# Kernel optimization log

Measured on AMD Instinct MI355X. Metric: run time of the kernel, lower is better.

Reference implementation:

```python
import jax, jax.numpy as jnp
import numpy as np

D = 1024
NH = 16
HD = D // NH
DFF = 4 * D
EPS = 1e-5


def setup_inputs() -> dict:
    key = jax.random.key(0)
    ks = jax.random.split(key, 12)
    s = lambda fan_in: 1.0 / np.sqrt(fan_in)
    return {
        "x": jax.random.normal(ks[0], (2, 2048, D), dtype=jnp.float32),
        # weights stored [in, out] (transpose of torch Linear layout)
        "w_qkv": jax.random.uniform(ks[1], (D, 3 * D), minval=-s(D), maxval=s(D)),
        "w_proj": jax.random.uniform(ks[2], (D, D), minval=-s(D), maxval=s(D)),
        "ln1_w": jnp.ones((D,), jnp.float32),
        "ln1_b": jnp.zeros((D,), jnp.float32),
        "ln2_w": jnp.ones((D,), jnp.float32),
        "ln2_b": jnp.zeros((D,), jnp.float32),
        "fc1_w": jax.random.uniform(ks[3], (D, DFF), minval=-s(D), maxval=s(D)),
        "fc1_b": jax.random.uniform(ks[4], (DFF,), minval=-s(D), maxval=s(D)),
        "fc2_w": jax.random.uniform(ks[5], (DFF, D), minval=-s(DFF), maxval=s(DFF)),
        "fc2_b": jax.random.uniform(ks[6], (D,), minval=-s(DFF), maxval=s(DFF)),
    }


def _layernorm(x, w, b):
    mu = jnp.mean(x, axis=-1, keepdims=True)
    var = jnp.mean(jnp.square(x - mu), axis=-1, keepdims=True)
    return (x - mu) * jax.lax.rsqrt(var + EPS) * w + b


def _attn(x, w_qkv, w_proj):
    B, T, C = x.shape
    qkv = x @ w_qkv  # [B,T,3C]
    q, k, v = jnp.split(qkv, 3, axis=-1)
    q = q.reshape(B, T, NH, HD).transpose(0, 2, 1, 3)  # [B,nh,T,hd]
    k = k.reshape(B, T, NH, HD).transpose(0, 2, 1, 3)
    v = v.reshape(B, T, NH, HD).transpose(0, 2, 1, 3)
    att = jnp.einsum("bhqd,bhkd->bhqk", q, k) / np.sqrt(HD)
    causal = jnp.tril(jnp.ones((T, T), bool))
    att = jnp.where(causal, att, -jnp.inf)
    att = jax.nn.softmax(att, axis=-1)
    out = jnp.einsum("bhqk,bhkd->bhqd", att, v)
    out = out.transpose(0, 2, 1, 3).reshape(B, T, C)
    return out @ w_proj


def reference(x, w_qkv, w_proj, ln1_w, ln1_b, ln2_w, ln2_b, fc1_w, fc1_b, fc2_w, fc2_b):
    x = x + _attn(_layernorm(x, ln1_w, ln1_b), w_qkv, w_proj)
    h = _layernorm(x, ln2_w, ln2_b)
    h = jax.nn.gelu(h @ fc1_w + fc1_b, approximate=False) @ fc2_w + fc2_b
    return x + h
```

## Files before the change

kernel.cpp:

```cpp
#include <hip/hip_runtime.h>


typedef short  bf16x8 __attribute__((ext_vector_type(8)));
typedef short  bf16x4 __attribute__((ext_vector_type(4)));
typedef float  fx4    __attribute__((ext_vector_type(4)));
typedef int    ix2    __attribute__((ext_vector_type(2)));

#define DEV static __device__ __forceinline__

DEV short f2bf(float f) {
    unsigned u = __builtin_bit_cast(unsigned, f);
    u += 0x7fffu + ((u >> 16) & 1u);
    return (short)(u >> 16);
}

#define AS1(p) ((__attribute__((address_space(1))) void*)(p))
#define AS3(p) ((__attribute__((address_space(3))) void*)(p))

__global__ __launch_bounds__(256) void ln_kernel(const float* __restrict__ x,
                                                 const float* __restrict__ w,
                                                 const float* __restrict__ b,
                                                 short* __restrict__ out)
{
    int row = blockIdx.x;
    int tid = threadIdx.x;
    const float4 v = *(const float4*)(x + (size_t)row * 1024 + tid * 4);
    float s = v.x + v.y + v.z + v.w;
    float q = v.x * v.x + v.y * v.y + v.z * v.z + v.w * v.w;
#pragma unroll
    for (int off = 32; off > 0; off >>= 1) {
        s += __shfl_down(s, off);
        q += __shfl_down(q, off);
    }
    __shared__ float ls[4], lq[4];
    if ((tid & 63) == 0) { ls[tid >> 6] = s; lq[tid >> 6] = q; }
    __syncthreads();
    float S  = ls[0] + ls[1] + ls[2] + ls[3];
    float Q  = lq[0] + lq[1] + lq[2] + lq[3];
    float mu  = S * (1.0f / 1024.0f);
    float var = Q * (1.0f / 1024.0f) - mu * mu;
    float inv = rsqrtf(var + 1e-5f);
    float4 wv = *(const float4*)(w + tid * 4);
    float4 bv = *(const float4*)(b + tid * 4);
    bf16x4 o;
    o[0] = f2bf((v.x - mu) * inv * wv.x + bv.x);
    o[1] = f2bf((v.y - mu) * inv * wv.y + bv.y);
    o[2] = f2bf((v.z - mu) * inv * wv.z + bv.z);
    o[3] = f2bf((v.w - mu) * inv * wv.w + bv.w);
    *(bf16x4*)(out + (size_t)row * 1024 + tid * 4) = o;
}

__global__ void transpose_f32_bf16(const float* __restrict__ in,
                                   short* __restrict__ out, int R, int C)
{
    __shared__ float tile[32][33];
    int c0 = blockIdx.x * 32, r0 = blockIdx.y * 32;
    int tx = threadIdx.x, ty = threadIdx.y;
#pragma unroll
    for (int dy = 0; dy < 32; dy += 8)
        tile[ty + dy][tx] = in[(size_t)(r0 + ty + dy) * C + c0 + tx];
    __syncthreads();
#pragma unroll
    for (int dy = 0; dy < 32; dy += 8)
        out[(size_t)(c0 + ty + dy) * R + r0 + tx] = f2bf(tile[tx][ty + dy]);
}

__global__ void vt_extract(const short* __restrict__ qkv, short* __restrict__ vt)
{
    __shared__ short tile[32][33];
    int t0 = blockIdx.x * 32, d0 = blockIdx.y * 32;
    int bh = blockIdx.z;
    int tx = threadIdx.x, ty = threadIdx.y;
    size_t inbase  = (size_t)(bh >> 4) * 2048 * 3072 + 2048 + (bh & 15) * 64;
    size_t outbase = (size_t)bh * 64 * 2048;
#pragma unroll
    for (int dy = 0; dy < 32; dy += 8)
        tile[ty + dy][tx] = qkv[inbase + (size_t)(t0 + ty + dy) * 3072 + d0 + tx];
    __syncthreads();
#pragma unroll
    for (int dy = 0; dy < 32; dy += 8)
        vt[outbase + (size_t)(d0 + ty + dy) * 2048 + t0 + tx] = tile[tx][ty + dy];
}

template <int BN, bool BIAS, bool GELU, bool RESID, bool OUT_BF16, bool PARTIAL>
__global__ __launch_bounds__(256) void gemm_bt(const short* __restrict__ A,
                                               const short* __restrict__ Bt,
                                               void* __restrict__ Cout,
                                               void* __restrict__ Cout2,
                                               const float* __restrict__ bias,
                                               const float* __restrict__ resid,
                                               int M, int N, int K)
{
    constexpr int NJ = BN / 32;
    __shared__ short As[2][128 * 32];
    __shared__ short Bs[2][BN * 32];
    int tid  = threadIdx.x;
    int lane = tid & 63, wv = tid >> 6;
    int quad = lane >> 4, l15 = lane & 15;
    int m0 = blockIdx.y * 128, n0 = blockIdx.x * BN;
    int SK   = gridDim.z;
    int kbeg = blockIdx.z * (K / SK);
    int NK   = (K / SK) / 32;
    int wr = (wv >> 1) * 64, wc = (wv & 1) * (BN / 2);
    fx4 acc[4][NJ] = {};
    int srow = lane >> 2;
    int scol = ((lane & 3) ^ (srow & 3)) * 8;
    int rg   = (quad ^ (l15 & 3)) * 8;
    const short* Ab = A  + (size_t)m0 * K;
    const short* Bb = Bt + (size_t)n0 * K;

    auto stage = [&](int buf, int k0) {
#pragma unroll
        for (int c = wv; c < 8; c += 4) {
            int row = c * 16 + srow;
            __builtin_amdgcn_global_load_lds(AS1(Ab + (size_t)row * K + k0 + scol),
                                             AS3(&As[buf][c * 512]), 16, 0, 0);
        }
#pragma unroll
        for (int c = wv; c < BN / 16; c += 4) {
            int row = c * 16 + srow;
            __builtin_amdgcn_global_load_lds(AS1(Bb + (size_t)row * K + k0 + scol),
                                             AS3(&Bs[buf][c * 512]), 16, 0, 0);
        }
    };

    stage(0, kbeg);
    __syncthreads();
    for (int kt = 0; kt < NK; ++kt) {
        int cur = kt & 1;
        if (kt + 1 < NK) stage(cur ^ 1, kbeg + (kt + 1) * 32);
        bf16x8 af[4], bfr[NJ];
#pragma unroll
        for (int i = 0; i < 4; ++i)
            af[i] = *(const bf16x8*)&As[cur][(wr + i * 16 + l15) * 32 + rg];
#pragma unroll
        for (int j = 0; j < NJ; ++j)
            bfr[j] = *(const bf16x8*)&Bs[cur][(wc + j * 16 + l15) * 32 + rg];
#pragma unroll
        for (int i = 0; i < 4; ++i)
#pragma unroll
            for (int j = 0; j < NJ; ++j)
                acc[i][j] = __builtin_amdgcn_mfma_f32_16x16x32_bf16(af[i], bfr[j], acc[i][j], 0, 0, 0);
        __syncthreads();
    }

    if constexpr (PARTIAL) {
        float* P = blockIdx.z ? (float*)Cout2 : (float*)Cout;
#pragma unroll
        for (int i = 0; i < 4; ++i)
#pragma unroll
            for (int j = 0; j < NJ; ++j)
#pragma unroll
                for (int r = 0; r < 4; ++r) {
                    int row = m0 + wr + i * 16 + quad * 4 + r;
                    int col = n0 + wc + j * 16 + l15;
                    P[(size_t)row * N + col] = acc[i][j][r];
                }
    } else {
#pragma unroll
        for (int i = 0; i < 4; ++i)
#pragma unroll
            for (int j = 0; j < NJ; ++j)
#pragma unroll
                for (int r = 0; r < 4; ++r) {
                    int row = m0 + wr + i * 16 + quad * 4 + r;
                    int col = n0 + wc + j * 16 + l15;
                    float v = acc[i][j][r];
                    if constexpr (BIAS)  v += bias[col];
                    if constexpr (GELU)  v = 0.5f * v * (1.0f + erff(v * 0.70710678118654752f));
                    if constexpr (RESID) v += resid[(size_t)row * N + col];
                    if constexpr (OUT_BF16) ((short*)Cout)[(size_t)row * N + col] = f2bf(v);
                    else                    ((float*)Cout)[(size_t)row * N + col] = v;
                }
    }
}

template <bool BIAS>
__global__ __launch_bounds__(256) void reduce2(const float* __restrict__ p0,
                                               const float* __restrict__ p1,
                                               const float* __restrict__ resid,
                                               const float* __restrict__ bias,
                                               float* __restrict__ out, int N)
{
    size_t idx = ((size_t)blockIdx.x * 256 + threadIdx.x) * 4;
    float4 a = *(const float4*)(p0 + idx);
    float4 b = *(const float4*)(p1 + idx);
    float4 r = *(const float4*)(resid + idx);
    float4 v;
    v.x = a.x + b.x + r.x; v.y = a.y + b.y + r.y;
    v.z = a.z + b.z + r.z; v.w = a.w + b.w + r.w;
    if constexpr (BIAS) {
        const float4 bv = *(const float4*)(bias + (idx & (N - 1)));
        v.x += bv.x; v.y += bv.y; v.z += bv.z; v.w += bv.w;
    }
    *(float4*)(out + idx) = v;
}

__global__ __launch_bounds__(256) void reduce2_ln(const float* __restrict__ p0,
                                                  const float* __restrict__ p1,
                                                  const float* __restrict__ resid,
                                                  const float* __restrict__ lw,
                                                  const float* __restrict__ lb,
                                                  float* __restrict__ out_f32,
                                                  short* __restrict__ out_bf16)
{
    int row = blockIdx.x, tid = threadIdx.x;
    size_t idx = (size_t)row * 1024 + tid * 4;
    float4 a = *(const float4*)(p0 + idx);
    float4 b = *(const float4*)(p1 + idx);
    float4 r = *(const float4*)(resid + idx);
    float4 v;
    v.x = a.x + b.x + r.x; v.y = a.y + b.y + r.y;
    v.z = a.z + b.z + r.z; v.w = a.w + b.w + r.w;
    *(float4*)(out_f32 + idx) = v;
    float s = v.x + v.y + v.z + v.w;
    float q = v.x * v.x + v.y * v.y + v.z * v.z + v.w * v.w;
#pragma unroll
    for (int off = 32; off > 0; off >>= 1) {
        s += __shfl_down(s, off);
        q += __shfl_down(q, off);
    }
    __shared__ float ls[4], lq[4];
    if ((tid & 63) == 0) { ls[tid >> 6] = s; lq[tid >> 6] = q; }
    __syncthreads();
    float S  = ls[0] + ls[1] + ls[2] + ls[3];
    float Q  = lq[0] + lq[1] + lq[2] + lq[3];
    float mu  = S * (1.0f / 1024.0f);
    float var = Q * (1.0f / 1024.0f) - mu * mu;
    float inv = rsqrtf(var + 1e-5f);
    float4 wv = *(const float4*)(lw + tid * 4);
    float4 bv = *(const float4*)(lb + tid * 4);
    bf16x4 o;
    o[0] = f2bf((v.x - mu) * inv * wv.x + bv.x);
    o[1] = f2bf((v.y - mu) * inv * wv.y + bv.y);
    o[2] = f2bf((v.z - mu) * inv * wv.z + bv.z);
    o[3] = f2bf((v.w - mu) * inv * wv.w + bv.w);
    *(bf16x4*)(out_bf16 + idx) = o;
}

__global__ __launch_bounds__(128) void attn_kernel(const short* __restrict__ qkv,
                                                   const short* __restrict__ vt,
                                                   short* __restrict__ out)
{
    __shared__ short Ks[2][64 * 64];
    __shared__ short Vs[2][64 * 64];
    const float CS = 0.125f * 1.44269504088896f;
    int tid  = threadIdx.x, lane = tid & 63, wv = tid >> 6;
    int quad = lane >> 4, l15 = lane & 15;
    int b = blockIdx.z, h = blockIdx.y, j = blockIdx.x;

    const short* kq = qkv + (size_t)b * 2048 * 3072 + 1024 + h * 64;
    const short* vb = vt  + (size_t)(b * 16 + h) * 64 * 2048;
    int srow = lane >> 3;
    int scol = ((lane & 7) ^ srow) * 8;
    int rg0  = (quad ^ (l15 & 7)) * 8;
    const bf16x4 vones = {(short)0x3F80, (short)0x3F80, (short)0x3F80, (short)0x3F80};

    for (int item = 0; item < 2; ++item) {
        int qt = item ? j : 63 - j;
        int q0 = qt * 32;
        int ktmax = qt >> 1;

        bf16x8 qf[2];
#pragma unroll
        for (int ks = 0; ks < 2; ++ks)
            qf[ks] = *(const bf16x8*)&qkv[(size_t)(b * 2048 + q0 + wv * 16 + l15) * 3072
                                           + h * 64 + ks * 32 + quad * 8];
        fx4 oacc[4] = {};
        fx4 lacc = {};

#pragma unroll
        for (int c = wv; c < 8; c += 2) {
            int row = c * 8 + srow;
            __builtin_amdgcn_global_load_lds(AS1(kq + (size_t)row * 3072 + scol),
                                             AS3(&Ks[0][c * 512]), 16, 0, 0);
            __builtin_amdgcn_global_load_lds(AS1(vb + (size_t)row * 2048 + scol),
                                             AS3(&Vs[0][c * 512]), 16, 0, 0);
        }
        __syncthreads();

        for (int kt = 0; kt <= ktmax; ++kt) {
            int cur = kt & 1;
            if (kt < ktmax) {
                int nb = cur ^ 1, tn = (kt + 1) * 64;
#pragma unroll
                for (int c = wv; c < 8; c += 2) {
                    int row = c * 8 + srow;
                    __builtin_amdgcn_global_load_lds(AS1(kq + (size_t)(tn + row) * 3072 + scol),
                                                     AS3(&Ks[nb][c * 512]), 16, 0, 0);
                    __builtin_amdgcn_global_load_lds(AS1(vb + (size_t)row * 2048 + tn + scol),
                                                     AS3(&Vs[nb][c * 512]), 16, 0, 0);
                }
            }

            fx4 s[4];
#pragma unroll
            for (int nt = 0; nt < 4; ++nt) {
                bf16x8 kf0 = *(const bf16x8*)&Ks[cur][(nt * 16 + l15) * 64 + rg0];
                bf16x8 kf1 = *(const bf16x8*)&Ks[cur][(nt * 16 + l15) * 64 + (rg0 ^ 32)];
                fx4 z = {0.f, 0.f, 0.f, 0.f};
                z = __builtin_amdgcn_mfma_f32_16x16x32_bf16(kf0, qf[0], z, 0, 0, 0);
                z = __builtin_amdgcn_mfma_f32_16x16x32_bf16(kf1, qf[1], z, 0, 0, 0);
                s[nt] = z;
            }
            if (kt == ktmax) {
                int delta = (qt & 1) * 32 + wv * 16 + l15;
#pragma unroll
                for (int nt = 0; nt < 4; ++nt)
#pragma unroll
                    for (int r = 0; r < 4; ++r)
                        if (nt * 16 + quad * 4 + r > delta) s[nt][r] = -1e30f;
            }

            bf16x4 pf[4];
#pragma unroll
            for (int nt = 0; nt < 4; ++nt) {
                float p0 = exp2f(s[nt][0] * CS);
                float p1 = exp2f(s[nt][1] * CS);
                float p2 = exp2f(s[nt][2] * CS);
                float p3 = exp2f(s[nt][3] * CS);
                unsigned a0 = __builtin_bit_cast(unsigned, p0) + 0x8000u;
                unsigned a1 = __builtin_bit_cast(unsigned, p1) + 0x8000u;
                unsigned a2 = __builtin_bit_cast(unsigned, p2) + 0x8000u;
                unsigned a3 = __builtin_bit_cast(unsigned, p3) + 0x8000u;
                ix2 pk;
                pk[0] = (int)__builtin_amdgcn_perm(a1, a0, 0x07060302u);
                pk[1] = (int)__builtin_amdgcn_perm(a3, a2, 0x07060302u);
                pf[nt] = __builtin_bit_cast(bf16x4, pk);
            }
#pragma unroll
            for (int nt = 0; nt < 4; ++nt)
                lacc = __builtin_amdgcn_mfma_f32_16x16x16bf16_1k(pf[nt], vones, lacc, 0, 0, 0);
#pragma unroll
            for (int dt = 0; dt < 4; ++dt) {
                int vrow  = dt * 16 + l15;
                int rbase = vrow * 64 + (quad & 1) * 4;
                int rk    = vrow & 7;
#pragma unroll
                for (int nt = 0; nt < 4; ++nt) {
                    int g = (nt * 2 + (quad >> 1)) ^ rk;
                    bf16x4 vf = *(const bf16x4*)&Vs[cur][rbase + g * 8];
                    oacc[dt] = __builtin_amdgcn_mfma_f32_16x16x16bf16_1k(pf[nt], vf, oacc[dt], 0, 0, 0);
                }
            }
            __syncthreads();
        }

        float linv[4];
#pragma unroll
        for (int r = 0; r < 4; ++r) linv[r] = 1.0f / lacc[r];
#pragma unroll
        for (int dt = 0; dt < 4; ++dt)
#pragma unroll
            for (int r = 0; r < 4; ++r) {
                int row = q0 + wv * 16 + quad * 4 + r;
                int col = h * 64 + dt * 16 + l15;
                out[((size_t)b * 2048 + row) * 1024 + col] = f2bf(oacc[dt][r] * linv[r]);
            }
    }
}

extern "C" void kernel_launch(void* const* d_in, const int* in_sizes, int n_in,
                              void* d_out, int out_size, void* d_ws, size_t ws_size,
                              hipStream_t stream)
{
    const float* x      = (const float*)d_in[0];
    const float* w_qkv  = (const float*)d_in[1];
    const float* w_proj = (const float*)d_in[2];
    const float* ln1_w  = (const float*)d_in[3];
    const float* ln1_b  = (const float*)d_in[4];
    const float* ln2_w  = (const float*)d_in[5];
    const float* ln2_b  = (const float*)d_in[6];
    const float* fc1_w  = (const float*)d_in[7];
    const float* fc1_b  = (const float*)d_in[8];
    const float* fc2_w  = (const float*)d_in[9];
    const float* fc2_b  = (const float*)d_in[10];
    float* out = (float*)d_out;
    char*  ws  = (char*)d_ws;

    size_t off = 0;
    auto alloc = [&](size_t bytes) { void* p = ws + off; off += (bytes + 255) & ~(size_t)255; return p; };
    short* tw_qkv  = (short*)alloc((size_t)3072 * 1024 * 2);
    short* tw_proj = (short*)alloc((size_t)1024 * 1024 * 2);
    short* tfc1    = (short*)alloc((size_t)4096 * 1024 * 2);
    short* tfc2    = (short*)alloc((size_t)1024 * 4096 * 2);
    short* xn      = (short*)alloc((size_t)4096 * 1024 * 2);
    short* qkvb    = (short*)alloc((size_t)4096 * 3072 * 2);
    short* vtb     = (short*)alloc((size_t)32 * 64 * 2048 * 2);
    short* attnb   = (short*)alloc((size_t)4096 * 1024 * 2);
    float* x1      = (float*)alloc((size_t)4096 * 1024 * 4);
    float* pk      = (float*)alloc((size_t)4096 * 1024 * 4);
    short* h1      = qkvb;

    dim3 tb(32, 8);
    transpose_f32_bf16<<<dim3(3072 / 32, 1024 / 32), tb, 0, stream>>>(w_qkv, tw_qkv, 1024, 3072);
    transpose_f32_bf16<<<dim3(1024 / 32, 1024 / 32), tb, 0, stream>>>(w_proj, tw_proj, 1024, 1024);
    transpose_f32_bf16<<<dim3(4096 / 32, 1024 / 32), tb, 0, stream>>>(fc1_w, tfc1, 1024, 4096);
    transpose_f32_bf16<<<dim3(1024 / 32, 4096 / 32), tb, 0, stream>>>(fc2_w, tfc2, 4096, 1024);

    ln_kernel<<<4096, 256, 0, stream>>>(x, ln1_w, ln1_b, xn);
    gemm_bt<128, false, false, false, true, false><<<dim3(24, 32, 1), 256, 0, stream>>>(
        xn, tw_qkv, qkvb, nullptr, nullptr, nullptr, 4096, 3072, 1024);
    vt_extract<<<dim3(2048 / 32, 64 / 32, 32), tb, 0, stream>>>(qkvb, vtb);
    attn_kernel<<<dim3(32, 16, 2), 128, 0, stream>>>(qkvb, vtb, attnb);
    gemm_bt<64, false, false, false, false, true><<<dim3(16, 32, 2), 256, 0, stream>>>(
        attnb, tw_proj, x1, pk, nullptr, nullptr, 4096, 1024, 1024);
    reduce2_ln<<<4096, 256, 0, stream>>>(x1, pk, x, ln2_w, ln2_b, x1, xn);
    gemm_bt<128, true, true, false, true, false><<<dim3(32, 32, 1), 256, 0, stream>>>(
        xn, tfc1, h1, nullptr, fc1_b, nullptr, 4096, 4096, 1024);
    gemm_bt<64, false, false, false, false, true><<<dim3(16, 32, 2), 256, 0, stream>>>(
        h1, tfc2, out, pk, nullptr, nullptr, 4096, 1024, 4096);
    reduce2<true><<<4096, 256, 0, stream>>>(out, pk, x1, fc2_b, out, 1024);
}
```

Baseline: 395.4 us.

## Vectorize weight transpose, change LDS swizzle, use sigmoid-based GELU approximation

```diff
diff --git a/kernel.cpp b/kernel.cpp
--- a/kernel.cpp
+++ b/kernel.cpp
@@ -50,19 +50,34 @@
     *(bf16x4*)(out + (size_t)row * 1024 + tid * 4) = o;
 }
 
-__global__ void transpose_f32_bf16(const float* __restrict__ in,
-                                   short* __restrict__ out, int R, int C)
-{
-    __shared__ float tile[32][33];
-    int c0 = blockIdx.x * 32, r0 = blockIdx.y * 32;
-    int tx = threadIdx.x, ty = threadIdx.y;
-#pragma unroll
-    for (int dy = 0; dy < 32; dy += 8)
-        tile[ty + dy][tx] = in[(size_t)(r0 + ty + dy) * C + c0 + tx];
+__global__ __launch_bounds__(256) void transpose_f32_bf16(const float* __restrict__ in,
+                                                          short* __restrict__ out,
+                                                          int R, int C)
+{
+    __shared__ float tile[64][65];
+    int c0 = blockIdx.x * 64, r0 = blockIdx.y * 64;
+    int t  = threadIdx.x;
+    int tx = t & 15, ty = t >> 4;
+#pragma unroll
+    for (int i = 0; i < 4; ++i) {
+        int row = i * 16 + ty;
+        float4 v = *(const float4*)(in + (size_t)(r0 + row) * C + c0 + tx * 4);
+        tile[row][tx * 4 + 0] = v.x;
+        tile[row][tx * 4 + 1] = v.y;
+        tile[row][tx * 4 + 2] = v.z;
+        tile[row][tx * 4 + 3] = v.w;
+    }
     __syncthreads();
-#pragma unroll
-    for (int dy = 0; dy < 32; dy += 8)
-        out[(size_t)(c0 + ty + dy) * R + r0 + tx] = f2bf(tile[tx][ty + dy]);
+    int seg = t & 7;
+#pragma unroll
+    for (int p = 0; p < 2; ++p) {
+        int orow = p * 32 + (t >> 3);
+        bf16x8 o;
+#pragma unroll
+        for (int u = 0; u < 8; ++u)
+            o[u] = f2bf(tile[seg * 8 + u][orow]);
+        *(bf16x8*)(out + (size_t)(c0 + orow) * R + r0 + seg * 8) = o;
+    }
 }
 
 __global__ void vt_extract(const short* __restrict__ qkv, short* __restrict__ vt)
@@ -104,8 +119,8 @@
     int wr = (wv >> 1) * 64, wc = (wv & 1) * (BN / 2);
     fx4 acc[4][NJ] = {};
     int srow = lane >> 2;
-    int scol = ((lane & 3) ^ (srow & 3)) * 8;
-    int rg   = (quad ^ (l15 & 3)) * 8;
+    int scol = ((lane & 3) ^ ((srow >> 1) & 3)) * 8;
+    int rg   = (quad ^ ((l15 >> 1) & 3)) * 8;
     const short* Ab = A  + (size_t)m0 * K;
     const short* Bb = Bt + (size_t)n0 * K;
 
@@ -167,7 +182,10 @@
                     int col = n0 + wc + j * 16 + l15;
                     float v = acc[i][j][r];
                     if constexpr (BIAS)  v += bias[col];
-                    if constexpr (GELU)  v = 0.5f * v * (1.0f + erff(v * 0.70710678118654752f));
+                    if constexpr (GELU) {
+                        float e = exp2f(v * -2.4554674f);
+                        v = v * __builtin_amdgcn_rcpf(1.0f + e);
+                    }
                     if constexpr (RESID) v += resid[(size_t)row * N + col];
                     if constexpr (OUT_BF16) ((short*)Cout)[(size_t)row * N + col] = f2bf(v);
                     else                    ((float*)Cout)[(size_t)row * N + col] = v;
@@ -392,16 +410,15 @@
     float* pk      = (float*)alloc((size_t)4096 * 1024 * 4);
     short* h1      = qkvb;
 
-    dim3 tb(32, 8);
-    transpose_f32_bf16<<<dim3(3072 / 32, 1024 / 32), tb, 0, stream>>>(w_qkv, tw_qkv, 1024, 3072);
-    transpose_f32_bf16<<<dim3(1024 / 32, 1024 / 32), tb, 0, stream>>>(w_proj, tw_proj, 1024, 1024);
-    transpose_f32_bf16<<<dim3(4096 / 32, 1024 / 32), tb, 0, stream>>>(fc1_w, tfc1, 1024, 4096);
-    transpose_f32_bf16<<<dim3(1024 / 32, 4096 / 32), tb, 0, stream>>>(fc2_w, tfc2, 4096, 1024);
+    transpose_f32_bf16<<<dim3(3072 / 64, 1024 / 64), 256, 0, stream>>>(w_qkv, tw_qkv, 1024, 3072);
+    transpose_f32_bf16<<<dim3(1024 / 64, 1024 / 64), 256, 0, stream>>>(w_proj, tw_proj, 1024, 1024);
+    transpose_f32_bf16<<<dim3(4096 / 64, 1024 / 64), 256, 0, stream>>>(fc1_w, tfc1, 1024, 4096);
+    transpose_f32_bf16<<<dim3(1024 / 64, 4096 / 64), 256, 0, stream>>>(fc2_w, tfc2, 4096, 1024);
 
     ln_kernel<<<4096, 256, 0, stream>>>(x, ln1_w, ln1_b, xn);
     gemm_bt<128, false, false, false, true, false><<<dim3(24, 32, 1), 256, 0, stream>>>(
         xn, tw_qkv, qkvb, nullptr, nullptr, nullptr, 4096, 3072, 1024);
-    vt_extract<<<dim3(2048 / 32, 64 / 32, 32), tb, 0, stream>>>(qkvb, vtb);
+    vt_extract<<<dim3(2048 / 32, 64 / 32, 32), dim3(32, 8), 0, stream>>>(qkvb, vtb);
     attn_kernel<<<dim3(32, 16, 2), 128, 0, stream>>>(qkvb, vtb, attnb);
     gemm_bt<64, false, false, false, false, true><<<dim3(16, 32, 2), 256, 0, stream>>>(
         attnb, tw_proj, x1, pk, nullptr, nullptr, 4096, 1024, 1024);
```

New measurement: 381.4 us. 3.6% less time.
